# Kernel tuning notes

Hardware: AMD Instinct MI355X
Metric: run time of the kernel (lower is better)

## Reference

```python
import jax, jax.numpy as jnp
import numpy as np
from jax import lax

# Model dims (match init_kwargs / Mamba2 defaults)
B = 8; C_IN = 512; C_OUT = 512; H = 32; W = 32; L = H * W
D_STATE = 64; D_CONV = 4; EXPAND = 2; HEADDIM = 64
D_INNER = EXPAND * C_IN            # 1024
NHEADS = D_INNER // HEADDIM        # 16
D_XBC = D_INNER + 2 * D_STATE      # 1152 (ngroups=1)
D_IN_PROJ = 2 * D_INNER + 2 * D_STATE + NHEADS
EPS = 1e-5


def setup_inputs() -> dict:
    key = jax.random.key(0)
    ks = jax.random.split(key, 16)
    x = jax.random.normal(ks[0], (B, C_IN, H, W), jnp.float32)
    ln_w = jnp.ones((C_IN,), jnp.float32)
    ln_b = jnp.zeros((C_IN,), jnp.float32)
    in_proj_w = jax.random.normal(ks[1], (D_IN_PROJ, C_IN), jnp.float32) * 0.02
    conv1d_w = jax.random.normal(ks[2], (D_XBC, D_CONV), jnp.float32) * 0.2
    conv1d_b = jax.random.normal(ks[3], (D_XBC,), jnp.float32) * 0.02
    dt0 = jax.random.uniform(ks[4], (NHEADS,), jnp.float32, 1e-3, 0.1)
    dt_bias = jnp.log(jnp.expm1(dt0))  # inverse softplus init
    A_log = jnp.log(jax.random.uniform(ks[5], (NHEADS,), jnp.float32, 1.0, 16.0))
    D = jax.random.normal(ks[6], (NHEADS,), jnp.float32)
    rms_w = jnp.ones((D_INNER,), jnp.float32)
    out_proj_w = jax.random.normal(ks[7], (C_IN, D_INNER), jnp.float32) * 0.02
    conv2d_w = jax.random.normal(ks[8], (C_OUT, C_IN), jnp.float32) * 0.04
    conv2d_b = jnp.zeros((C_OUT,), jnp.float32)
    bn_g = jnp.ones((C_OUT,), jnp.float32)
    bn_b = jnp.zeros((C_OUT,), jnp.float32)
    bn_mean = jnp.zeros((C_OUT,), jnp.float32)
    bn_var = jnp.ones((C_OUT,), jnp.float32)
    return dict(x=x, ln_w=ln_w, ln_b=ln_b, in_proj_w=in_proj_w, conv1d_w=conv1d_w,
                conv1d_b=conv1d_b, dt_bias=dt_bias, A_log=A_log, D=D, rms_w=rms_w,
                out_proj_w=out_proj_w, conv2d_w=conv2d_w, conv2d_b=conv2d_b,
                bn_g=bn_g, bn_b=bn_b, bn_mean=bn_mean, bn_var=bn_var)


def reference(x, ln_w, ln_b, in_proj_w, conv1d_w, conv1d_b, dt_bias, A_log, D,
              rms_w, out_proj_w, conv2d_w, conv2d_b, bn_g, bn_b, bn_mean, bn_var):
    Bb, C, Hh, Ww = x.shape
    Ltok = Hh * Ww
    # tokens: (B, L, C)
    t = x.reshape(Bb, C, Ltok).transpose(0, 2, 1)
    # LayerNorm over channel dim
    mu = jnp.mean(t, -1, keepdims=True)
    var = jnp.mean(jnp.square(t - mu), -1, keepdims=True)
    xn = (t - mu) * lax.rsqrt(var + EPS) * ln_w + ln_b
    # Mamba2 in_proj -> [z, xBC, dt]
    zxbcdt = jnp.einsum('blc,dc->bld', xn, in_proj_w)
    z = zxbcdt[..., :D_INNER]
    xBC = zxbcdt[..., D_INNER:D_INNER + D_XBC]
    dt = zxbcdt[..., D_INNER + D_XBC:]                       # (B, L, nheads)
    # causal depthwise conv1d + silu
    conv = lax.conv_general_dilated(xBC.transpose(0, 2, 1), conv1d_w[:, None, :],
                                    window_strides=(1,), padding=[(D_CONV - 1, 0)],
                                    feature_group_count=D_XBC)
    xBC = jax.nn.silu(conv.transpose(0, 2, 1) + conv1d_b)
    xh = xBC[..., :D_INNER].reshape(Bb, Ltok, NHEADS, HEADDIM)
    Bm = xBC[..., D_INNER:D_INNER + D_STATE]                 # (B, L, d_state)
    Cm = xBC[..., D_INNER + D_STATE:]
    dt = jax.nn.softplus(dt + dt_bias)
    A = -jnp.exp(A_log)                                      # (nheads,)
    # selective scan (SSD recurrence), state h: (B, nheads, headdim, d_state)
    def step(h, inp):
        xt, dtt, Bt, Ct = inp
        dA = jnp.exp(dtt * A)                                # (B, nheads)
        h = h * dA[..., None, None] + jnp.einsum('bh,bhp,bs->bhps', dtt, xt, Bt)
        y = jnp.einsum('bhps,bs->bhp', h, Ct)
        return h, y
    h0 = jnp.zeros((Bb, NHEADS, HEADDIM, D_STATE), x.dtype)
    xs = (xh.transpose(1, 0, 2, 3), dt.transpose(1, 0, 2),
          Bm.transpose(1, 0, 2), Cm.transpose(1, 0, 2))
    _, ys = lax.scan(step, h0, xs)
    y = ys.transpose(1, 0, 2, 3) + D[None, None, :, None] * xh
    y = y.reshape(Bb, Ltok, D_INNER)
    # gated RMSNorm
    y = y * jax.nn.silu(z)
    y = y * lax.rsqrt(jnp.mean(y * y, -1, keepdims=True) + EPS) * rms_w
    out = jnp.einsum('bld,cd->blc', y, out_proj_w)
    img = out.transpose(0, 2, 1).reshape(Bb, C, Hh, Ww)
    # 1x1 conv + BN (inference) + ReLU
    c = jnp.einsum('bchw,oc->bohw', img, conv2d_w) + conv2d_b[None, :, None, None]
    c = (c - bn_mean[None, :, None, None]) * lax.rsqrt(bn_var + EPS)[None, :, None, None]
    c = c * bn_g[None, :, None, None] + bn_b[None, :, None, None]
    return jax.nn.relu(c)
```

## Files before the change

kernel.cpp:

```cpp
#include <hip/hip_runtime.h>
#include <hip/hip_bf16.h>

#define NB 8
#define LL 1024
#define CIN 512
#define DIN 1024
#define DXBC 1152
#define DPROJ 2192
#define NPADW 2304
#define NHH 16
#define HDD 64
#define DST 64
#define NCHUNK 16
#define QCH 64
#define XBCS 1024
#define CTT 8
#define DTB 16

typedef unsigned short u16;
typedef unsigned int u32;
typedef __bf16 bf16x8 __attribute__((ext_vector_type(8)));
typedef float f32x4 __attribute__((ext_vector_type(4)));
typedef u16 u16x8 __attribute__((ext_vector_type(8)));

__device__ __forceinline__ float bf2f(u16 u) {
    u32 x = ((u32)u) << 16; float f; __builtin_memcpy(&f, &x, 4); return f;
}
__device__ __forceinline__ u16 f2bf(float f) {
    u32 x; __builtin_memcpy(&x, &f, 4);
    u32 r = x + 0x7fff + ((x >> 16) & 1);
    return (u16)(r >> 16);
}

__device__ __forceinline__ void gload16(const u16* g, u16* l) {
    __builtin_amdgcn_global_load_lds((__attribute__((address_space(1))) void*)(g),
                                     (__attribute__((address_space(3))) void*)(l), 16, 0, 0);
}

__device__ __forceinline__ int swz(int row, int cb) {
    return row * 64 + ((cb ^ ((row & 7) << 4)) >> 1);
}

__global__ void f2bf_kernel(const float* __restrict__ s, u16* __restrict__ d, int n) {
    int i = blockIdx.x * 256 + threadIdx.x;
    if (i < n) d[i] = f2bf(s[i]);
}
__global__ void f2bf_pad(const float* __restrict__ s, u16* __restrict__ d, int nsrc, int ndst) {
    int i = blockIdx.x * 256 + threadIdx.x;
    if (i < ndst) d[i] = (i < nsrc) ? f2bf(s[i]) : (u16)0;
}
__global__ __launch_bounds__(256) void woutT_conv(const float* __restrict__ s,
                                                  const float* __restrict__ rw,
                                                  u16* __restrict__ dt) {
    __shared__ float tile[64][65];
    int bc = blockIdx.x & 7, bd = blockIdx.x >> 3;
    int c0 = bc * 64, d0 = bd * 64;
    int t = threadIdx.x;
    int r4 = t >> 6, cc = t & 63;
#pragma unroll
    for (int rr = 0; rr < 16; ++rr) {
        int row = r4 * 16 + rr;
        tile[row][cc] = s[(size_t)(c0 + row) * DIN + d0 + cc];
    }
    __syncthreads();
#pragma unroll
    for (int rr = 0; rr < 16; ++rr) {
        int row = r4 * 16 + rr;
        dt[(size_t)(d0 + row) * CIN + c0 + cc] = f2bf(tile[cc][row] * rw[d0 + row]);
    }
}
__global__ void bn_prep(const float* __restrict__ cb, const float* __restrict__ g,
                        const float* __restrict__ bb, const float* __restrict__ mean,
                        const float* __restrict__ var, float* __restrict__ scale,
                        float* __restrict__ shift) {
    int i = blockIdx.x * 256 + threadIdx.x;
    if (i < CIN) {
        float rs = rsqrtf(var[i] + 1e-5f);
        float sc = g[i] * rs;
        scale[i] = sc;
        shift[i] = (cb[i] - mean[i]) * sc + bb[i];
    }
}

__global__ __launch_bounds__(256) void ln_kernel(const float* __restrict__ x,
                                                 const float* __restrict__ lw,
                                                 const float* __restrict__ lb,
                                                 u16* __restrict__ xn) {
    __shared__ u16 tile[CIN * 33];
    __shared__ float psum[8][32], psq[8][32], muA[32], rsA[32];
    int bid = blockIdx.x;
    int b = bid >> 5, hw0 = (bid & 31) * 32;
    int t = threadIdx.x;
    int hw = t & 31, cg = t >> 5;
    const float* xb = x + (size_t)b * CIN * LL + hw0 + hw;
    float s = 0.f, sq = 0.f;
    for (int r = 0; r < CIN / 8; ++r) {
        int c = r * 8 + cg;
        float v = xb[(size_t)c * LL];
        s += v; sq += v * v;
        tile[c * 33 + hw] = f2bf(v);
    }
    psum[cg][hw] = s; psq[cg][hw] = sq;
    __syncthreads();
    if (t < 32) {
        float ss = 0.f, qq = 0.f;
        for (int g = 0; g < 8; ++g) { ss += psum[g][t]; qq += psq[g][t]; }
        float mu = ss * (1.f / CIN);
        float var = qq * (1.f / CIN) - mu * mu;
        muA[t] = mu; rsA[t] = rsqrtf(var + 1e-5f);
    }
    __syncthreads();
    for (int r = 0; r < 64; ++r) {
        int idx = r * 256 + t;
        int c = idx & (CIN - 1);
        int hh = idx >> 9;
        float v = (bf2f(tile[c * 33 + hh]) - muA[hh]) * rsA[hh] * lw[c] + lb[c];
        xn[((size_t)(b * LL + hw0 + hh)) * CIN + c] = f2bf(v);
    }
}

template <int EPI>
__global__ __launch_bounds__(256) void gemm_bt(const u16* __restrict__ A, const u16* __restrict__ Bw,
                                               void* __restrict__ Cout, int M, int N, int K, int ldc,
                                               int nx,
                                               const float* __restrict__ scale,
                                               const float* __restrict__ shift,
                                               const float* __restrict__ rsc) {
    __shared__ u16 As[2][128 * 64], Bs[2][128 * 64];
    int t = threadIdx.x;
    int lane = t & 63, wave = t >> 6;
    int nblk = gridDim.x;
    int qq = nblk >> 3, rm = nblk & 7;
    int xcd = blockIdx.x & 7, idx = blockIdx.x >> 3;
    int swzb = (xcd < rm ? xcd * (qq + 1) : rm * (qq + 1) + (xcd - rm) * qq) + idx;
    int m0 = (swzb / nx) * 128, n0 = (swzb % nx) * 128;
    int wr = wave >> 1, wc = wave & 1;
    f32x4 acc[4][4];
    for (int m = 0; m < 4; ++m)
        for (int n = 0; n < 4; ++n)
            for (int q = 0; q < 4; ++q) acc[m][n][q] = 0.f;

    const u16* Arow = A + (size_t)m0 * K;
    const u16* Brow = Bw + (size_t)n0 * K;
    int s4 = lane >> 4;
    int rr = lane & 15;

    auto STAGE = [&](int buf, int k0) {
#pragma unroll
        for (int j = 0; j < 4; ++j) {
            int e = j * 256 + t;
            int r = e >> 3, sr = e & 7;
            int src = (sr ^ (r & 7)) * 8;
            gload16(Arow + (size_t)r * K + k0 + src, &As[buf][e * 8]);
            gload16(Brow + (size_t)r * K + k0 + src, &Bs[buf][e * 8]);
        }
    };

    STAGE(0, 0);
    int NK = K >> 6, cur = 0;
    for (int kt = 0; kt < NK; ++kt) {
        if (kt + 1 < NK) {
            STAGE(cur ^ 1, (kt + 1) << 6);
            asm volatile("s_waitcnt vmcnt(8)" ::: "memory");
        } else {
            asm volatile("s_waitcnt vmcnt(0)" ::: "memory");
        }
        __builtin_amdgcn_s_barrier();
        __builtin_amdgcn_sched_barrier(0);
#pragma unroll
        for (int kk = 0; kk < 2; ++kk) {
            bf16x8 af[4], bfr[4];
#pragma unroll
            for (int m = 0; m < 4; ++m) {
                int row = wr * 64 + m * 16 + rr;
                int ss = (kk * 4 + s4) ^ (row & 7);
                af[m] = *(const bf16x8*)&As[cur][row * 64 + ss * 8];
            }
#pragma unroll
            for (int n = 0; n < 4; ++n) {
                int row = wc * 64 + n * 16 + rr;
                int ss = (kk * 4 + s4) ^ (row & 7);
                bfr[n] = *(const bf16x8*)&Bs[cur][row * 64 + ss * 8];
            }
#pragma unroll
            for (int m = 0; m < 4; ++m)
#pragma unroll
                for (int n = 0; n < 4; ++n)
                    acc[m][n] = __builtin_amdgcn_mfma_f32_16x16x32_bf16(af[m], bfr[n], acc[m][n], 0, 0, 0);
        }
        __builtin_amdgcn_s_barrier();
        cur ^= 1;
    }
    int fq = lane >> 4, fr = lane & 15;
#pragma unroll
    for (int m = 0; m < 4; ++m) {
#pragma unroll
        for (int n = 0; n < 4; ++n) {
            int col = n0 + wc * 64 + n * 16 + fr;
#pragma unroll
            for (int q = 0; q < 4; ++q) {
                int row = m0 + wr * 64 + m * 16 + fq * 4 + q;
                float v = acc[m][n][q];
                if (EPI == 0) {
                    ((u16*)Cout)[(size_t)row * ldc + col] = f2bf(v);
                } else {
                    v = v * rsc[col];
                    v = v * scale[row] + shift[row];
                    v = v > 0.f ? v : 0.f;
                    ((float*)Cout)[((size_t)(col >> 10)) * (CIN * LL) + (size_t)row * LL + (col & 1023)] = v;
                }
            }
        }
    }
}

__global__ __launch_bounds__(288) void conv1d_fused(const u16* __restrict__ zx,
                                                    const float* __restrict__ w,
                                                    const float* __restrict__ bias,
                                                    u16* __restrict__ xbc,
                                                    float* __restrict__ Bc, float* __restrict__ Cc) {
    int bid = blockIdx.x;
    int b = bid >> 7;
    int l0 = (bid & 127) * CTT;
    int t = threadIdx.x;
    bool isX = t < 256;
    int ch = isX ? t * 4 : 1024 + (t - 256) * 4;

    float4 wv0 = *(const float4*)&w[(ch + 0) * 4];
    float4 wv1 = *(const float4*)&w[(ch + 1) * 4];
    float4 wv2 = *(const float4*)&w[(ch + 2) * 4];
    float4 wv3 = *(const float4*)&w[(ch + 3) * 4];
    float4 bv = *(const float4*)&bias[ch];

    ushort4 xin[CTT + 3];
    const u16* src = zx + (size_t)(b * LL + l0 - 3) * NPADW + DIN + ch;
#pragma unroll
    for (int i = 0; i < CTT + 3; ++i) {
        ushort4 v = {0, 0, 0, 0};
        if (l0 + i - 3 >= 0) v = *(const ushort4*)(src + (size_t)i * NPADW);
        xin[i] = v;
    }
#pragma unroll
    for (int i = 0; i < CTT; ++i) {
        int tok = b * LL + l0 + i;
        float a0 = bv.x + bf2f(xin[i].x) * wv0.x + bf2f(xin[i + 1].x) * wv0.y +
                   bf2f(xin[i + 2].x) * wv0.z + bf2f(xin[i + 3].x) * wv0.w;
        float a1 = bv.y + bf2f(xin[i].y) * wv1.x + bf2f(xin[i + 1].y) * wv1.y +
                   bf2f(xin[i + 2].y) * wv1.z + bf2f(xin[i + 3].y) * wv1.w;
        float a2 = bv.z + bf2f(xin[i].z) * wv2.x + bf2f(xin[i + 1].z) * wv2.y +
                   bf2f(xin[i + 2].z) * wv2.z + bf2f(xin[i + 3].z) * wv2.w;
        float a3 = bv.w + bf2f(xin[i].w) * wv3.x + bf2f(xin[i + 1].w) * wv3.y +
                   bf2f(xin[i + 2].w) * wv3.z + bf2f(xin[i + 3].w) * wv3.w;
        float s0 = a0 / (1.f + __expf(-a0));
        float s1 = a1 / (1.f + __expf(-a1));
        float s2 = a2 / (1.f + __expf(-a2));
        float s3 = a3 / (1.f + __expf(-a3));
        if (isX) {
            ushort4 o;
            o.x = f2bf(s0); o.y = f2bf(s1); o.z = f2bf(s2); o.w = f2bf(s3);
            *(ushort4*)&xbc[(size_t)tok * XBCS + ch] = o;
        } else {
            int s = ch - 1024;
            float4 o4; o4.x = s0; o4.y = s1; o4.z = s2; o4.w = s3;
            if (s < DST) *(float4*)&Bc[(size_t)tok * DST + s] = o4;
            else         *(float4*)&Cc[(size_t)tok * DST + (s - DST)] = o4;
        }
    }
}

__global__ __launch_bounds__(256) void dt_gemv(const u16* __restrict__ xn,
                                               const float* __restrict__ wproj,
                                               const float* __restrict__ dt_bias,
                                               const float* __restrict__ A_log,
                                               float2* __restrict__ dtda) {
    int t = threadIdx.x;
    int h = t >> 4, part = t & 15;
    int tok0 = blockIdx.x * DTB;
    const float* wr = wproj + (size_t)(DIN + DXBC + h) * CIN + part * 32;
    float4 w[8];
#pragma unroll
    for (int i = 0; i < 8; ++i) w[i] = *(const float4*)&wr[i * 4];
    const float* wf = (const float*)w;
    float dtb = dt_bias[h];
    float An = -__expf(A_log[h]);
#pragma unroll
    for (int tl = 0; tl < DTB; ++tl) {
        int tok = tok0 + tl;
        const u16* xr = xn + (size_t)tok * CIN + part * 32;
        u16x8 xv0 = *(const u16x8*)&xr[0];
        u16x8 xv1 = *(const u16x8*)&xr[8];
        u16x8 xv2 = *(const u16x8*)&xr[16];
        u16x8 xv3 = *(const u16x8*)&xr[24];
        float s = 0.f;
#pragma unroll
        for (int i = 0; i < 8; ++i) s += bf2f(xv0[i]) * wf[i];
#pragma unroll
        for (int i = 0; i < 8; ++i) s += bf2f(xv1[i]) * wf[8 + i];
#pragma unroll
        for (int i = 0; i < 8; ++i) s += bf2f(xv2[i]) * wf[16 + i];
#pragma unroll
        for (int i = 0; i < 8; ++i) s += bf2f(xv3[i]) * wf[24 + i];
        s += __shfl_xor(s, 1, 64);
        s += __shfl_xor(s, 2, 64);
        s += __shfl_xor(s, 4, 64);
        s += __shfl_xor(s, 8, 64);
        if (part == 0) {
            float si = s + dtb;
            float dtv = si > 15.f ? si : __logf(1.f + __expf(si));
            float2 dd; dd.x = dtv; dd.y = dtv * An;
            dtda[(size_t)tok * NHH + h] = dd;
        }
    }
}

__global__ __launch_bounds__(256) void ssd_chunk(const float* __restrict__ Bcb,
                                                 const float* __restrict__ Ccb,
                                                 const u16* __restrict__ xbc,
                                                 const float2* __restrict__ dtda,
                                                 u16* __restrict__ yi,
                                                 u16* __restrict__ DHb,
                                                 u16* __restrict__ C2G,
                                                 float* __restrict__ DC) {
    __shared__ u16 Bt[4096], Ct[4096], XT[4096], BTt[4096], Gt[4096];
    __shared__ float Sar[64], dtvA[64], wA[64], eSA[64];
    int tau = blockIdx.x;
    int b = tau >> 8, h = (tau >> 4) & 15, c = tau & 15;
    int t0g = b * LL + c * QCH;
    int t = threadIdx.x, lane = t & 63, wave = t >> 6;
    int row = t >> 2, q = t & 3;

    {
        const float* bp = Bcb + (size_t)(t0g + row) * DST + q * 16;
        const float* cp = Ccb + (size_t)(t0g + row) * DST + q * 16;
#pragma unroll
        for (int half = 0; half < 2; ++half) {
            float4 v0 = *(const float4*)(bp + half * 8);
            float4 v1 = *(const float4*)(bp + half * 8 + 4);
            u16x8 o;
            o[0] = f2bf(v0.x); o[1] = f2bf(v0.y); o[2] = f2bf(v0.z); o[3] = f2bf(v0.w);
            o[4] = f2bf(v1.x); o[5] = f2bf(v1.y); o[6] = f2bf(v1.z); o[7] = f2bf(v1.w);
            *(u16x8*)&Bt[swz(row, q * 32 + half * 16)] = o;
            float4 c0 = *(const float4*)(cp + half * 8);
            float4 c1 = *(const float4*)(cp + half * 8 + 4);
            u16x8 oc;
            oc[0] = f2bf(c0.x); oc[1] = f2bf(c0.y); oc[2] = f2bf(c0.z); oc[3] = f2bf(c0.w);
            oc[4] = f2bf(c1.x); oc[5] = f2bf(c1.y); oc[6] = f2bf(c1.z); oc[7] = f2bf(c1.w);
            *(u16x8*)&Ct[swz(row, q * 32 + half * 16)] = oc;
        }
        const u16* xp = xbc + (size_t)(t0g + row) * XBCS + h * HDD + q * 16;
        u16x8 x0 = *(const u16x8*)xp;
        u16x8 x1 = *(const u16x8*)(xp + 8);
#pragma unroll
        for (int e = 0; e < 8; ++e) XT[swz(q * 16 + e, row * 2)] = x0[e];
#pragma unroll
        for (int e = 0; e < 8; ++e) XT[swz(q * 16 + 8 + e, row * 2)] = x1[e];
    }
    if (t < 64) {
        float2 dd = dtda[(size_t)(t0g + t) * NHH + h];
        float s = dd.y;
#pragma unroll
        for (int off = 1; off < 64; off <<= 1) {
            float u = __shfl_up(s, off, 64);
            if (t >= off) s += u;
        }
        float SQ = __shfl(s, 63, 64);
        Sar[t] = s; dtvA[t] = dd.x;
        wA[t] = __expf(SQ - s) * dd.x;
        eSA[t] = __expf(s);
        if (t == 0) DC[tau] = __expf(SQ);
    }
    __syncthreads();

    int R = wave >> 1, Cq = wave & 1, rr = lane & 15, sg = lane >> 4;
    f32x4 g[2][2];
#pragma unroll
    for (int mi = 0; mi < 2; ++mi)
#pragma unroll
        for (int ni = 0; ni < 2; ++ni)
#pragma unroll
            for (int r = 0; r < 4; ++r) g[mi][ni][r] = 0.f;
#pragma unroll
    for (int kt = 0; kt < 2; ++kt) {
        int cb = kt * 64 + sg * 16;
        bf16x8 a0 = *(const bf16x8*)&Ct[swz(R * 32 + rr, cb)];
        bf16x8 a1 = *(const bf16x8*)&Ct[swz(R * 32 + 16 + rr, cb)];
        bf16x8 b0 = *(const bf16x8*)&Bt[swz(Cq * 32 + rr, cb)];
        bf16x8 b1 = *(const bf16x8*)&Bt[swz(Cq * 32 + 16 + rr, cb)];
        g[0][0] = __builtin_amdgcn_mfma_f32_16x16x32_bf16(a0, b0, g[0][0], 0, 0, 0);
        g[0][1] = __builtin_amdgcn_mfma_f32_16x16x32_bf16(a0, b1, g[0][1], 0, 0, 0);
        g[1][0] = __builtin_amdgcn_mfma_f32_16x16x32_bf16(a1, b0, g[1][0], 0, 0, 0);
        g[1][1] = __builtin_amdgcn_mfma_f32_16x16x32_bf16(a1, b1, g[1][1], 0, 0, 0);
    }
#pragma unroll
    for (int mi = 0; mi < 2; ++mi)
#pragma unroll
        for (int ni = 0; ni < 2; ++ni)
#pragma unroll
            for (int r = 0; r < 4; ++r) {
                int i = R * 32 + mi * 16 + sg * 4 + r;
                int j = Cq * 32 + ni * 16 + rr;
                float v = (i >= j) ? g[mi][ni][r] * __expf(Sar[i] - Sar[j]) * dtvA[j] : 0.f;
                Gt[swz(i, j * 2)] = f2bf(v);
            }
#pragma unroll
    for (int half = 0; half < 2; ++half) {
        u16x8 cv = *(const u16x8*)&Ct[swz(row, q * 32 + half * 16)];
        u16x8 ov;
#pragma unroll
        for (int e = 0; e < 8; ++e) ov[e] = f2bf(bf2f(cv[e]) * eSA[row]);
        *(u16x8*)&C2G[(size_t)tau * 4096 + row * 64 + q * 16 + half * 8] = ov;
        u16x8 bv = *(const u16x8*)&Bt[swz(row, q * 32 + half * 16)];
#pragma unroll
        for (int e = 0; e < 8; ++e)
            BTt[swz(q * 16 + half * 8 + e, row * 2)] = f2bf(bf2f(bv[e]) * wA[row]);
    }
    __syncthreads();

    f32x4 y[2][2], dh[2][2];
#pragma unroll
    for (int mi = 0; mi < 2; ++mi)
#pragma unroll
        for (int ni = 0; ni < 2; ++ni)
#pragma unroll
            for (int r = 0; r < 4; ++r) { y[mi][ni][r] = 0.f; dh[mi][ni][r] = 0.f; }
#pragma unroll
    for (int kt = 0; kt < 2; ++kt) {
        int cb = kt * 64 + sg * 16;
        bf16x8 xb0 = *(const bf16x8*)&XT[swz(Cq * 32 + rr, cb)];
        bf16x8 xb1 = *(const bf16x8*)&XT[swz(Cq * 32 + 16 + rr, cb)];
        bf16x8 ga0 = *(const bf16x8*)&Gt[swz(R * 32 + rr, cb)];
        bf16x8 ga1 = *(const bf16x8*)&Gt[swz(R * 32 + 16 + rr, cb)];
        bf16x8 ba0 = *(const bf16x8*)&BTt[swz(R * 32 + rr, cb)];
        bf16x8 ba1 = *(const bf16x8*)&BTt[swz(R * 32 + 16 + rr, cb)];
        y[0][0] = __builtin_amdgcn_mfma_f32_16x16x32_bf16(ga0, xb0, y[0][0], 0, 0, 0);
        y[0][1] = __builtin_amdgcn_mfma_f32_16x16x32_bf16(ga0, xb1, y[0][1], 0, 0, 0);
        y[1][0] = __builtin_amdgcn_mfma_f32_16x16x32_bf16(ga1, xb0, y[1][0], 0, 0, 0);
        y[1][1] = __builtin_amdgcn_mfma_f32_16x16x32_bf16(ga1, xb1, y[1][1], 0, 0, 0);
        dh[0][0] = __builtin_amdgcn_mfma_f32_16x16x32_bf16(ba0, xb0, dh[0][0], 0, 0, 0);
        dh[0][1] = __builtin_amdgcn_mfma_f32_16x16x32_bf16(ba0, xb1, dh[0][1], 0, 0, 0);
        dh[1][0] = __builtin_amdgcn_mfma_f32_16x16x32_bf16(ba1, xb0, dh[1][0], 0, 0, 0);
        dh[1][1] = __builtin_amdgcn_mfma_f32_16x16x32_bf16(ba1, xb1, dh[1][1], 0, 0, 0);
    }
#pragma unroll
    for (int mi = 0; mi < 2; ++mi)
#pragma unroll
        for (int ni = 0; ni < 2; ++ni)
#pragma unroll
            for (int r = 0; r < 4; ++r) {
                int i = R * 32 + mi * 16 + sg * 4 + r;
                int p = Cq * 32 + ni * 16 + rr;
                yi[(size_t)(t0g + i) * DIN + h * HDD + p] = f2bf(y[mi][ni][r]);
                DHb[(size_t)tau * 4096 + i * 64 + p] = f2bf(dh[mi][ni][r]);
            }
}

__global__ __launch_bounds__(256) void ssd_carry(const u16* __restrict__ DHb,
                                                 const float* __restrict__ DC,
                                                 u16* __restrict__ HPREV) {
    int bid = blockIdx.x;
    int bh = bid >> 1, ph = bid & 1;
    int t = threadIdx.x;
    int s = t >> 2, p0 = ph * 32 + (t & 3) * 8;
    size_t base = (size_t)bh * NCHUNK * 4096 + s * 64 + p0;
    float Hv[8] = {0.f, 0.f, 0.f, 0.f, 0.f, 0.f, 0.f, 0.f};
    for (int c = 0; c < NCHUNK; ++c) {
        size_t off = base + (size_t)c * 4096;
        u16x8 hp;
#pragma unroll
        for (int e = 0; e < 8; ++e) hp[e] = f2bf(Hv[e]);
        *(u16x8*)&HPREV[off] = hp;
        float d = DC[bh * NCHUNK + c];
        u16x8 dv = *(const u16x8*)&DHb[off];
#pragma unroll
        for (int e = 0; e < 8; ++e) Hv[e] = d * Hv[e] + bf2f(dv[e]);
    }
}

__global__ __launch_bounds__(256) void ssd_final(const u16* __restrict__ C2G,
                                                 const u16* __restrict__ HPREV,
                                                 const u16* __restrict__ xbc,
                                                 const u16* __restrict__ zx,
                                                 const float* __restrict__ Dp,
                                                 u16* __restrict__ yi) {
    __shared__ u16 C2t[4096], HT[4096];
    int tau = blockIdx.x;
    int b = tau >> 8, h = (tau >> 4) & 15, c = tau & 15;
    int t0g = b * LL + c * QCH;
    int t = threadIdx.x, lane = t & 63, wave = t >> 6;
    int row = t >> 2, q = t & 3;
#pragma unroll
    for (int half = 0; half < 2; ++half) {
        u16x8 cv = *(const u16x8*)&C2G[(size_t)tau * 4096 + row * 64 + q * 16 + half * 8];
        *(u16x8*)&C2t[swz(row, q * 32 + half * 16)] = cv;
        u16x8 hv = *(const u16x8*)&HPREV[(size_t)tau * 4096 + row * 64 + q * 16 + half * 8];
#pragma unroll
        for (int e = 0; e < 8; ++e) HT[swz(q * 16 + half * 8 + e, row * 2)] = hv[e];
    }
    __syncthreads();
    int R = wave >> 1, Cq = wave & 1, rr = lane & 15, sg = lane >> 4;
    float Dh = Dp[h];
    f32x4 acc[2][2];
#pragma unroll
    for (int mi = 0; mi < 2; ++mi)
#pragma unroll
        for (int ni = 0; ni < 2; ++ni)
#pragma unroll
            for (int r = 0; r < 4; ++r) {
                int i = R * 32 + mi * 16 + sg * 4 + r;
                int p = Cq * 32 + ni * 16 + rr;
                acc[mi][ni][r] = bf2f(yi[(size_t)(t0g + i) * DIN + h * HDD + p]);
            }
#pragma unroll
    for (int kt = 0; kt < 2; ++kt) {
        int cb = kt * 64 + sg * 16;
        bf16x8 a0 = *(const bf16x8*)&C2t[swz(R * 32 + rr, cb)];
        bf16x8 a1 = *(const bf16x8*)&C2t[swz(R * 32 + 16 + rr, cb)];
        bf16x8 b0 = *(const bf16x8*)&HT[swz(Cq * 32 + rr, cb)];
        bf16x8 b1 = *(const bf16x8*)&HT[swz(Cq * 32 + 16 + rr, cb)];
        acc[0][0] = __builtin_amdgcn_mfma_f32_16x16x32_bf16(a0, b0, acc[0][0], 0, 0, 0);
        acc[0][1] = __builtin_amdgcn_mfma_f32_16x16x32_bf16(a0, b1, acc[0][1], 0, 0, 0);
        acc[1][0] = __builtin_amdgcn_mfma_f32_16x16x32_bf16(a1, b0, acc[1][0], 0, 0, 0);
        acc[1][1] = __builtin_amdgcn_mfma_f32_16x16x32_bf16(a1, b1, acc[1][1], 0, 0, 0);
    }
#pragma unroll
    for (int mi = 0; mi < 2; ++mi)
#pragma unroll
        for (int ni = 0; ni < 2; ++ni)
#pragma unroll
            for (int r = 0; r < 4; ++r) {
                int i = R * 32 + mi * 16 + sg * 4 + r;
                int p = Cq * 32 + ni * 16 + rr;
                size_t tok = t0g + i;
                int col = h * HDD + p;
                float xf = bf2f(xbc[tok * XBCS + col]);
                float zf = bf2f(zx[tok * NPADW + col]);
                float yo = (acc[mi][ni][r] + Dh * xf) * (zf / (1.f + __expf(-zf)));
                yi[tok * DIN + col] = f2bf(yo);
            }
}

__global__ __launch_bounds__(256) void rs_kernel(const u16* __restrict__ y,
                                                 float* __restrict__ rs) {
    int row = blockIdx.x, t = threadIdx.x;
    ushort4 uv = *(const ushort4*)&y[(size_t)row * DIN + t * 4];
    float v0 = bf2f(uv.x), v1 = bf2f(uv.y), v2 = bf2f(uv.z), v3 = bf2f(uv.w);
    float ss = v0 * v0 + v1 * v1 + v2 * v2 + v3 * v3;
#pragma unroll
    for (int o = 1; o < 64; o <<= 1) ss += __shfl_xor(ss, o, 64);
    __shared__ float ps[4];
    if ((t & 63) == 0) ps[t >> 6] = ss;
    __syncthreads();
    if (t == 0) {
        float tot = ps[0] + ps[1] + ps[2] + ps[3];
        rs[row] = rsqrtf(tot * (1.f / DIN) + 1e-5f);
    }
}

extern "C" void kernel_launch(void* const* d_in, const int* in_sizes, int n_in,
                              void* d_out, int out_size, void* d_ws, size_t ws_size,
                              hipStream_t stream) {
    const float* x         = (const float*)d_in[0];
    const float* ln_w      = (const float*)d_in[1];
    const float* ln_b      = (const float*)d_in[2];
    const float* in_proj_w = (const float*)d_in[3];
    const float* conv1d_w  = (const float*)d_in[4];
    const float* conv1d_b  = (const float*)d_in[5];
    const float* dt_bias   = (const float*)d_in[6];
    const float* A_log     = (const float*)d_in[7];
    const float* Dp        = (const float*)d_in[8];
    const float* rms_w     = (const float*)d_in[9];
    const float* out_proj_w= (const float*)d_in[10];
    const float* conv2d_w  = (const float*)d_in[11];
    const float* conv2d_b  = (const float*)d_in[12];
    const float* bn_g      = (const float*)d_in[13];
    const float* bn_b      = (const float*)d_in[14];
    const float* bn_mean   = (const float*)d_in[15];
    const float* bn_var    = (const float*)d_in[16];

    const int TOK = NB * LL;
    const int NTAU = NB * NHH * NCHUNK;
    char* ws = (char*)d_ws;
    size_t off = 0;
    auto alloc = [&](size_t bytes) {
        void* p = ws + off;
        off += (bytes + 255) & ~(size_t)255;
        return p;
    };
    u16*   Win   = (u16*)alloc((size_t)NPADW * CIN * 2);
    u16*   WoutT = (u16*)alloc((size_t)DIN * CIN * 2);
    u16*   Wc2   = (u16*)alloc((size_t)CIN * CIN * 2);
    u16*   WCMB  = (u16*)alloc((size_t)CIN * DIN * 2);
    u16*   XN    = (u16*)alloc((size_t)TOK * CIN * 2);
    u16*   ZX    = (u16*)alloc((size_t)TOK * NPADW * 2);
    u16*   XBC   = (u16*)alloc((size_t)TOK * XBCS * 2);
    float* Bcb   = (float*)alloc((size_t)TOK * DST * 4);
    float* Ccb   = (float*)alloc((size_t)TOK * DST * 4);
    float2* DTDA = (float2*)alloc((size_t)TOK * NHH * 8);
    u16*   YI    = (u16*)alloc((size_t)TOK * DIN * 2);
    u16*   DHb   = (u16*)alloc((size_t)NTAU * 4096 * 2);
    u16*   C2G   = (u16*)alloc((size_t)NTAU * 4096 * 2);
    u16*   HPREV = (u16*)alloc((size_t)NTAU * 4096 * 2);
    float* DC    = (float*)alloc((size_t)NTAU * 4);
    float* RS    = (float*)alloc((size_t)TOK * 4);
    float* BNSC  = (float*)alloc(CIN * 4);
    float* BNSH  = (float*)alloc(CIN * 4);

    f2bf_pad<<<(NPADW * CIN + 255) / 256, 256, 0, stream>>>(in_proj_w, Win, DPROJ * CIN, NPADW * CIN);
    woutT_conv<<<128, 256, 0, stream>>>(out_proj_w, rms_w, WoutT);
    f2bf_kernel<<<(CIN * CIN + 255) / 256, 256, 0, stream>>>(conv2d_w, Wc2, CIN * CIN);
    bn_prep<<<2, 256, 0, stream>>>(conv2d_b, bn_g, bn_b, bn_mean, bn_var, BNSC, BNSH);
    gemm_bt<0><<<(CIN / 128) * (DIN / 128), 256, 0, stream>>>(Wc2, WoutT, WCMB, CIN, DIN, CIN, DIN,
                                                              DIN / 128, nullptr, nullptr, nullptr);

    ln_kernel<<<256, 256, 0, stream>>>(x, ln_w, ln_b, XN);

    gemm_bt<0><<<(TOK / 128) * (NPADW / 128), 256, 0, stream>>>(XN, Win, ZX, TOK, NPADW, CIN, NPADW,
                                                                NPADW / 128, nullptr, nullptr, nullptr);

    conv1d_fused<<<NB * (LL / CTT), 288, 0, stream>>>(ZX, conv1d_w, conv1d_b, XBC, Bcb, Ccb);
    dt_gemv<<<TOK / DTB, 256, 0, stream>>>(XN, in_proj_w, dt_bias, A_log, DTDA);

    ssd_chunk<<<NTAU, 256, 0, stream>>>(Bcb, Ccb, XBC, DTDA, YI, DHb, C2G, DC);
    ssd_carry<<<256, 256, 0, stream>>>(DHb, DC, HPREV);
    ssd_final<<<NTAU, 256, 0, stream>>>(C2G, HPREV, XBC, ZX, Dp, YI);

    rs_kernel<<<TOK, 256, 0, stream>>>(YI, RS);

    gemm_bt<1><<<(CIN / 128) * (TOK / 128), 256, 0, stream>>>(WCMB, YI, d_out, CIN, TOK, DIN, 0,
                                                              TOK / 128, BNSC, BNSH, RS);
}
```

Baseline: 167.2 us.

## Fuse RMS sum-of-squares into ssd_final and recompute scaled C instead of storing it

ssd_chunk no longer writes a scaled bf16 C matrix per chunk. It stores only the per-row exp(cumsum) factors, and ssd_final rebuilds the scaled C from the fp32 C buffer. ssd_final also accumulates per-token partial sums of squares of the gated output, and a small kernel reduces them across heads into the RMS scale. This removes the separate rs_kernel pass that reread all of YI, plus the C2G round trip. In exchange ssd_final reads fp32 C, which is wider than the bf16 buffer it replaces, and does an extra reduction with a sync. The sum of squares now uses fp32 values before bf16 rounding, a small numeric difference.

Result: faster. 161.5 us (-3.4%).

```diff
diff --git a/kernel.cpp b/kernel.cpp
--- a/kernel.cpp
+++ b/kernel.cpp
@@ -319,10 +319,10 @@
                                                  const float2* __restrict__ dtda,
                                                  u16* __restrict__ yi,
                                                  u16* __restrict__ DHb,
-                                                 u16* __restrict__ C2G,
+                                                 float* __restrict__ ESA,
                                                  float* __restrict__ DC) {
     __shared__ u16 Bt[4096], Ct[4096], XT[4096], BTt[4096], Gt[4096];
-    __shared__ float Sar[64], dtvA[64], wA[64], eSA[64];
+    __shared__ float Sar[64], dtvA[64], wA[64];
     int tau = blockIdx.x;
     int b = tau >> 8, h = (tau >> 4) & 15, c = tau & 15;
     int t0g = b * LL + c * QCH;
@@ -366,7 +366,7 @@
         float SQ = __shfl(s, 63, 64);
         Sar[t] = s; dtvA[t] = dd.x;
         wA[t] = __expf(SQ - s) * dd.x;
-        eSA[t] = __expf(s);
+        ESA[(size_t)tau * 64 + t] = __expf(s);
         if (t == 0) DC[tau] = __expf(SQ);
     }
     __syncthreads();
@@ -404,11 +404,6 @@
             }
 #pragma unroll
     for (int half = 0; half < 2; ++half) {
-        u16x8 cv = *(const u16x8*)&Ct[swz(row, q * 32 + half * 16)];
-        u16x8 ov;
-#pragma unroll
-        for (int e = 0; e < 8; ++e) ov[e] = f2bf(bf2f(cv[e]) * eSA[row]);
-        *(u16x8*)&C2G[(size_t)tau * 4096 + row * 64 + q * 16 + half * 8] = ov;
         u16x8 bv = *(const u16x8*)&Bt[swz(row, q * 32 + half * 16)];
 #pragma unroll
         for (int e = 0; e < 8; ++e)
@@ -476,25 +471,38 @@
     }
 }
 
-__global__ __launch_bounds__(256) void ssd_final(const u16* __restrict__ C2G,
+__global__ __launch_bounds__(256) void ssd_final(const float* __restrict__ Ccb,
+                                                 const float* __restrict__ ESA,
                                                  const u16* __restrict__ HPREV,
                                                  const u16* __restrict__ xbc,
                                                  const u16* __restrict__ zx,
                                                  const float* __restrict__ Dp,
-                                                 u16* __restrict__ yi) {
+                                                 u16* __restrict__ yi,
+                                                 float* __restrict__ PS) {
     __shared__ u16 C2t[4096], HT[4096];
+    __shared__ float smem_ps[2][64];
     int tau = blockIdx.x;
     int b = tau >> 8, h = (tau >> 4) & 15, c = tau & 15;
     int t0g = b * LL + c * QCH;
     int t = threadIdx.x, lane = t & 63, wave = t >> 6;
     int row = t >> 2, q = t & 3;
-#pragma unroll
-    for (int half = 0; half < 2; ++half) {
-        u16x8 cv = *(const u16x8*)&C2G[(size_t)tau * 4096 + row * 64 + q * 16 + half * 8];
-        *(u16x8*)&C2t[swz(row, q * 32 + half * 16)] = cv;
-        u16x8 hv = *(const u16x8*)&HPREV[(size_t)tau * 4096 + row * 64 + q * 16 + half * 8];
-#pragma unroll
-        for (int e = 0; e < 8; ++e) HT[swz(q * 16 + half * 8 + e, row * 2)] = hv[e];
+    {
+        float esa = ESA[(size_t)tau * 64 + row];
+        const float* cp = Ccb + (size_t)(t0g + row) * DST + q * 16;
+#pragma unroll
+        for (int half = 0; half < 2; ++half) {
+            float4 c0 = *(const float4*)(cp + half * 8);
+            float4 c1 = *(const float4*)(cp + half * 8 + 4);
+            u16x8 oc;
+            oc[0] = f2bf(c0.x * esa); oc[1] = f2bf(c0.y * esa);
+            oc[2] = f2bf(c0.z * esa); oc[3] = f2bf(c0.w * esa);
+            oc[4] = f2bf(c1.x * esa); oc[5] = f2bf(c1.y * esa);
+            oc[6] = f2bf(c1.z * esa); oc[7] = f2bf(c1.w * esa);
+            *(u16x8*)&C2t[swz(row, q * 32 + half * 16)] = oc;
+            u16x8 hv = *(const u16x8*)&HPREV[(size_t)tau * 4096 + row * 64 + q * 16 + half * 8];
+#pragma unroll
+            for (int e = 0; e < 8; ++e) HT[swz(q * 16 + half * 8 + e, row * 2)] = hv[e];
+        }
     }
     __syncthreads();
     int R = wave >> 1, Cq = wave & 1, rr = lane & 15, sg = lane >> 4;
@@ -522,6 +530,11 @@
         acc[1][0] = __builtin_amdgcn_mfma_f32_16x16x32_bf16(a1, b0, acc[1][0], 0, 0, 0);
         acc[1][1] = __builtin_amdgcn_mfma_f32_16x16x32_bf16(a1, b1, acc[1][1], 0, 0, 0);
     }
+    float ps[2][4];
+#pragma unroll
+    for (int mi = 0; mi < 2; ++mi)
+#pragma unroll
+        for (int r = 0; r < 4; ++r) ps[mi][r] = 0.f;
 #pragma unroll
     for (int mi = 0; mi < 2; ++mi)
 #pragma unroll
@@ -536,24 +549,33 @@
                 float zf = bf2f(zx[tok * NPADW + col]);
                 float yo = (acc[mi][ni][r] + Dh * xf) * (zf / (1.f + __expf(-zf)));
                 yi[tok * DIN + col] = f2bf(yo);
+                ps[mi][r] += yo * yo;
             }
-}
-
-__global__ __launch_bounds__(256) void rs_kernel(const u16* __restrict__ y,
-                                                 float* __restrict__ rs) {
-    int row = blockIdx.x, t = threadIdx.x;
-    ushort4 uv = *(const ushort4*)&y[(size_t)row * DIN + t * 4];
-    float v0 = bf2f(uv.x), v1 = bf2f(uv.y), v2 = bf2f(uv.z), v3 = bf2f(uv.w);
-    float ss = v0 * v0 + v1 * v1 + v2 * v2 + v3 * v3;
-#pragma unroll
-    for (int o = 1; o < 64; o <<= 1) ss += __shfl_xor(ss, o, 64);
-    __shared__ float ps[4];
-    if ((t & 63) == 0) ps[t >> 6] = ss;
+#pragma unroll
+    for (int mi = 0; mi < 2; ++mi)
+#pragma unroll
+        for (int r = 0; r < 4; ++r) {
+            float s2 = ps[mi][r];
+            s2 += __shfl_xor(s2, 1, 64);
+            s2 += __shfl_xor(s2, 2, 64);
+            s2 += __shfl_xor(s2, 4, 64);
+            s2 += __shfl_xor(s2, 8, 64);
+            if (rr == 0) smem_ps[Cq][R * 32 + mi * 16 + sg * 4 + r] = s2;
+        }
     __syncthreads();
-    if (t == 0) {
-        float tot = ps[0] + ps[1] + ps[2] + ps[3];
-        rs[row] = rsqrtf(tot * (1.f / DIN) + 1e-5f);
-    }
+    if (t < 64) PS[(size_t)tau * 64 + t] = smem_ps[0][t] + smem_ps[1][t];
+}
+
+__global__ __launch_bounds__(256) void rs_from_ps(const float* __restrict__ PS,
+                                                  float* __restrict__ RS) {
+    int tok = blockIdx.x * 256 + threadIdx.x;
+    int b = tok >> 10, rem = tok & 1023;
+    int c = rem >> 6, i = rem & 63;
+    float s = 0.f;
+#pragma unroll
+    for (int h = 0; h < NHH; ++h)
+        s += PS[(size_t)(((b << 4) + h) * 16 + c) * 64 + i];
+    RS[tok] = rsqrtf(s * (1.f / DIN) + 1e-5f);
 }
 
 extern "C" void kernel_launch(void* const* d_in, const int* in_sizes, int n_in,
@@ -598,8 +620,9 @@
     float2* DTDA = (float2*)alloc((size_t)TOK * NHH * 8);
     u16*   YI    = (u16*)alloc((size_t)TOK * DIN * 2);
     u16*   DHb   = (u16*)alloc((size_t)NTAU * 4096 * 2);
-    u16*   C2G   = (u16*)alloc((size_t)NTAU * 4096 * 2);
     u16*   HPREV = (u16*)alloc((size_t)NTAU * 4096 * 2);
+    float* ESA   = (float*)alloc((size_t)NTAU * 64 * 4);
+    float* PS    = (float*)alloc((size_t)NTAU * 64 * 4);
     float* DC    = (float*)alloc((size_t)NTAU * 4);
     float* RS    = (float*)alloc((size_t)TOK * 4);
     float* BNSC  = (float*)alloc(CIN * 4);
@@ -620,11 +643,11 @@
     conv1d_fused<<<NB * (LL / CTT), 288, 0, stream>>>(ZX, conv1d_w, conv1d_b, XBC, Bcb, Ccb);
     dt_gemv<<<TOK / DTB, 256, 0, stream>>>(XN, in_proj_w, dt_bias, A_log, DTDA);
 
-    ssd_chunk<<<NTAU, 256, 0, stream>>>(Bcb, Ccb, XBC, DTDA, YI, DHb, C2G, DC);
+    ssd_chunk<<<NTAU, 256, 0, stream>>>(Bcb, Ccb, XBC, DTDA, YI, DHb, ESA, DC);
     ssd_carry<<<256, 256, 0, stream>>>(DHb, DC, HPREV);
-    ssd_final<<<NTAU, 256, 0, stream>>>(C2G, HPREV, XBC, ZX, Dp, YI);
-
-    rs_kernel<<<TOK, 256, 0, stream>>>(YI, RS);
+    ssd_final<<<NTAU, 256, 0, stream>>>(Ccb, ESA, HPREV, XBC, ZX, Dp, YI, PS);
+
+    rs_from_ps<<<TOK / 256, 256, 0, stream>>>(PS, RS);
 
     gemm_bt<1><<<(CIN / 128) * (TOK / 128), 256, 0, stream>>>(WCMB, YI, d_out, CIN, TOK, DIN, 0,
                                                               TOK / 128, BNSC, BNSH, RS);
```
